# Kernel optimization log

Measured on AMD Instinct MI355X. Metric: run time of the kernel, lower is better.

The kernel has to match this reference:

```python
import jax, jax.numpy as jnp
import numpy as np

H = 12  # num_heads (init kwarg)


def setup_inputs() -> dict:
    key = jax.random.key(0)
    ks = jax.random.split(key, 9)
    B, S, D, M = 2, 1025, 768, 4
    hw = S - 1
    x = jax.random.normal(ks[0], (B, S, D), dtype=jnp.float32)
    masks = jax.random.randint(ks[1], (B, M, hw), 0, 2, dtype=jnp.int32)
    init = lambda k: jax.random.normal(k, (D, D), dtype=jnp.float32) * 0.02
    return {
        'x': x, 'masks': masks,
        'Wq': init(ks[2]), 'bq': jnp.zeros((D,), jnp.float32),
        'Wk': init(ks[3]), 'bk': jnp.zeros((D,), jnp.float32),
        'Wv': init(ks[4]), 'bv': jnp.zeros((D,), jnp.float32),
    }


def reference(x, masks, Wq, bq, Wk, bk, Wv, bv):
    B, S, D = x.shape
    hd = D // H
    scale = 1.0 / jnp.sqrt(jnp.asarray(hd, x.dtype))

    def heads(t):  # (B,S,D) -> (B,H,S,hd)
        return t.reshape(B, S, H, hd).transpose(0, 2, 1, 3)

    q = heads(x @ Wq.T + bq)
    k = heads(x @ Wk.T + bk)
    v = heads(x @ Wv.T + bv)

    scores_ori = jnp.einsum('bhqd,bhkd->bhqk', q, k) * scale  # (B,H,S,S)
    attn = jax.nn.softmax(scores_ori, axis=-1)  # dropout is identity at eval
    h = jnp.einsum('bhqk,bhkd->bhqd', attn, v)
    h = h.transpose(0, 2, 1, 3).reshape(B, S, D)

    # ---- mask-expanded attention (torch.no_grad branch) ----
    Mk, hw = masks.shape[1], masks.shape[2]
    m = masks.astype(x.dtype)  # (B,M,hw)
    # pad: position 0 (CLS) gets 0, positions 1..hw get the mask
    new_masks = jnp.pad(m, ((0, 0), (0, 0), (1, S - 1 - hw)))  # (B,M,S)
    bias = -10000.0 * (1.0 - new_masks)  # additive mask bias
    new_scores = scores_ori[:, None] + bias[:, :, None, None, :]  # (B,M,H,S,S)
    new_attn = jax.nn.softmax(new_scores, axis=-1)
    new_h = jnp.einsum('bmhqk,bhkd->bmhqd', new_attn, v)  # v repeated per mask
    new_h = new_h.transpose(0, 1, 3, 2, 4).reshape(B * Mk, S, D)

    img_idx = jnp.repeat(jnp.arange(B), Mk)  # [0]*M + [1]*M + ...
    new_x = jnp.broadcast_to(x[:, None], (B, Mk, S, D)).reshape(B * Mk, S, D)
    return (h, new_h, img_idx, new_x)
```

## Files before the change

### kernel.cpp

```cpp
#include <hip/hip_runtime.h>

typedef float f32x4 __attribute__((ext_vector_type(4)));
typedef short s16x8 __attribute__((ext_vector_type(8)));

constexpr int B  = 2;
constexpr int S  = 1025;
constexpr int D  = 768;
constexpr int DD = D * D;
constexpr int H  = 12;
constexpr int NM = 4;
constexpr int ROWS = B * S;
constexpr int BSD  = B * S * D;
constexpr int KPAD = 1088;
constexpr int NHB  = B * H;
constexpr int NQT  = 65;
constexpr int NKT  = 17;
constexpr int NV5  = 5;
constexpr int NATT = NHB * NQT;
constexpr int NCPY = 512;
constexpr int OUT_NEWH_OFF = BSD;
constexpr int OUT_IDX_OFF  = BSD + NM * BSD;
constexpr int OUT_NEWX_OFF = OUT_IDX_OFF + B * NM;

#define QSCALE 0.18033688011112042f

constexpr size_t QF_SZ = (size_t)NHB * NQT * 2 * 512;
constexpr size_t KF_SZ = (size_t)NHB * NKT * 4 * 2 * 512;
constexpr size_t VF_SZ = KF_SZ;

__device__ __forceinline__ unsigned short f2bf(float f) {
    unsigned u = __builtin_bit_cast(unsigned, f);
    u += 0x7FFF + ((u >> 16) & 1);
    return (unsigned short)(u >> 16);
}

__device__ __forceinline__ void gll16(const void* g, void* l) {
    __builtin_amdgcn_global_load_lds(
        (const __attribute__((address_space(1))) void*)g,
        (__attribute__((address_space(3))) void*)l, 16, 0, 0);
}

__global__ __launch_bounds__(256) void conv_kernel(
    const float* __restrict__ x, const float* __restrict__ Wq,
    const float* __restrict__ Wk, const float* __restrict__ Wv,
    const int* __restrict__ masks,
    unsigned short* __restrict__ xb, unsigned short* __restrict__ Wb,
    unsigned short* __restrict__ Mmb,
    unsigned short* __restrict__ Qf, unsigned short* __restrict__ Kf,
    unsigned short* __restrict__ Vf)
{
    constexpr int NX8 = BSD / 8;
    constexpr int NW8 = DD / 8;
    constexpr int TOT = NX8 + 3 * NW8;
    const int stride = gridDim.x * 256;
    const int tid = blockIdx.x * 256 + threadIdx.x;
    for (int c = tid; c < TOT; c += stride) {
        const float* src;
        unsigned short* dst;
        if (c < NX8) { src = x + (size_t)c * 8; dst = xb + (size_t)c * 8; }
        else {
            const int cc = c - NX8;
            const int mt = cc / NW8;
            const int rr = cc - mt * NW8;
            src = ((mt == 0) ? Wq : (mt == 1) ? Wk : Wv) + (size_t)rr * 8;
            dst = Wb + (size_t)mt * DD + (size_t)rr * 8;
        }
        const float4 a = *(const float4*)src;
        const float4 b2 = *(const float4*)(src + 4);
        s16x8 v;
        v[0] = (short)f2bf(a.x);  v[1] = (short)f2bf(a.y);
        v[2] = (short)f2bf(a.z);  v[3] = (short)f2bf(a.w);
        v[4] = (short)f2bf(b2.x); v[5] = (short)f2bf(b2.y);
        v[6] = (short)f2bf(b2.z); v[7] = (short)f2bf(b2.w);
        *(s16x8*)dst = v;
    }
    if (tid < B * NV5 * KPAD) {
        const int k    = tid % KPAD;
        const int rest = tid / KPAD;
        const int vv   = rest % NV5;
        const int bb   = rest / NV5;
        unsigned short m;
        if (vv == 0) m = (k < S) ? 0xFFFFu : 0u;
        else m = (k >= 1 && k < S &&
                  masks[(size_t)(bb * NM + vv - 1) * (S - 1) + k - 1]) ? 0xFFFFu : 0u;
        Mmb[tid] = m;
    }
    constexpr int KZ = NHB * 8 * 512;
    for (int i = tid; i < KZ; i += stride) {
        const int hb = i >> 12, off = i & 4095;
        Kf[(((size_t)(hb * NKT + NKT - 1)) << 12) + off] = 0;
        Vf[(((size_t)(hb * NKT + NKT - 1)) << 12) + off] = 0;
    }
    constexpr int QZ = NHB * 2 * 512;
    for (int i = tid; i < QZ; i += stride) {
        const int hb = i >> 10, off = i & 1023;
        Qf[(((size_t)(hb * NQT + NQT - 1) * 2) << 9) + off] = 0;
    }
}

__global__ __launch_bounds__(256, 2) void qkv_mfma_kernel(
    const unsigned short* __restrict__ xb, const unsigned short* __restrict__ Wb,
    const float* __restrict__ bq, const float* __restrict__ bk,
    const float* __restrict__ bv,
    unsigned short* __restrict__ Qf, unsigned short* __restrict__ Kf,
    unsigned short* __restrict__ Vf)
{
    __shared__ __align__(16) unsigned short Xs[2][128 * 64];
    __shared__ __align__(16) unsigned short Wl[2][128 * 64];

    const int t = threadIdx.x;
    const int row0 = blockIdx.x * 128;
    const int cy = blockIdx.y;
    const int mt = cy / 6;
    const int col0 = (cy % 6) * 128;
    const float* bias = (mt == 0) ? bq : (mt == 1) ? bk : bv;
    const unsigned short* Wsrc = Wb + (size_t)mt * DD;

    const int w = t >> 6, l = t & 63, lq = l & 15, grp = l >> 4;
    const int wr = w >> 1, wc = w & 1;

    auto stage = [&](int buf, int k0) {
        #pragma unroll
        for (int i = 0; i < 4; ++i) {
            const int slot = i * 256 + t;
            const int r = slot >> 3, cl = slot & 7;
            const int cg = cl ^ (r & 7);
            int row = row0 + r; if (row > ROWS - 1) row = ROWS - 1;
            gll16(xb + (size_t)row * D + k0 + cg * 8, &Xs[buf][slot * 8]);
            gll16(Wsrc + (size_t)(col0 + r) * D + k0 + cg * 8, &Wl[buf][slot * 8]);
        }
    };

    f32x4 acc[4][4] = {};
    stage(0, 0);

    for (int ks = 0; ks < 12; ++ks) {
        const int cur = ks & 1;
        __syncthreads();
        if (ks + 1 < 12) stage(cur ^ 1, (ks + 1) * 64);

        s16x8 a[4][2], bf[4][2];
        #pragma unroll
        for (int i = 0; i < 4; ++i) {
            const int xr = wr * 64 + i * 16 + lq;
            #pragma unroll
            for (int kh = 0; kh < 2; ++kh)
                a[i][kh] = *(const s16x8*)&Xs[cur][xr * 64 + (((kh * 4 + grp) ^ (xr & 7)) * 8)];
        }
        #pragma unroll
        for (int j = 0; j < 4; ++j) {
            const int wrow = wc * 64 + j * 16 + lq;
            #pragma unroll
            for (int kh = 0; kh < 2; ++kh)
                bf[j][kh] = *(const s16x8*)&Wl[cur][wrow * 64 + (((kh * 4 + grp) ^ (wrow & 7)) * 8)];
        }
        #pragma unroll
        for (int i = 0; i < 4; ++i)
            #pragma unroll
            for (int j = 0; j < 4; ++j) {
                acc[i][j] = __builtin_amdgcn_mfma_f32_16x16x32_bf16(a[i][0], bf[j][0], acc[i][j], 0, 0, 0);
                acc[i][j] = __builtin_amdgcn_mfma_f32_16x16x32_bf16(a[i][1], bf[j][1], acc[i][j], 0, 0, 0);
            }
    }

    #pragma unroll
    for (int j = 0; j < 4; ++j) {
        const int col = col0 + wc * 64 + j * 16 + lq;
        const float bv_ = bias[col];
        #pragma unroll
        for (int i = 0; i < 4; ++i) {
            #pragma unroll
            for (int r = 0; r < 4; ++r) {
                const int row = row0 + wr * 64 + i * 16 + grp * 4 + r;
                if (row >= ROWS) continue;
                const float raw = acc[i][j][r] + bv_;
                const int bb = (row >= S) ? 1 : 0;
                const int s  = row - bb * S;
                const int hb2 = bb * H + (col >> 6);
                const int d   = col & 63;
                if (mt == 0) {
                    const size_t idx = (((size_t)(hb2 * NQT + (s >> 4)) * 2 + (d >> 5)) << 9)
                                     + (((((d >> 3) & 3) << 4) + (s & 15)) << 3) + (d & 7);
                    Qf[idx] = f2bf(raw * QSCALE);
                } else if (mt == 1) {
                    const size_t idx = ((((size_t)(hb2 * NKT + (s >> 6)) * 4 + ((s >> 4) & 3)) * 2 + (d >> 5)) << 9)
                                     + (((((d >> 3) & 3) << 4) + (s & 15)) << 3) + (d & 7);
                    Kf[idx] = f2bf(raw);
                } else {
                    const int kk = s & 63;
                    const size_t idx = ((((size_t)(hb2 * NKT + (s >> 6)) * 4 + (d >> 4)) * 2 + (kk >> 5)) << 9)
                                     + (((((kk >> 3) & 3) << 4) + (d & 15)) << 3) + (kk & 7);
                    Vf[idx] = f2bf(raw);
                }
            }
        }
    }
}

__global__ __launch_bounds__(384) void attn_mfma_kernel(
    const unsigned short* __restrict__ Qf, const unsigned short* __restrict__ Kf,
    const unsigned short* __restrict__ Vf, const unsigned short* __restrict__ Mmb,
    const float* __restrict__ x,
    float* __restrict__ out_h, float* __restrict__ out_newh,
    float* __restrict__ out_newx, float* __restrict__ out_idx)
{
    if (blockIdx.x >= NATT) {
        const int cb = blockIdx.x - NATT;
        const int SLAB4  = S * D / 4;
        const int TOTAL4 = B * NM * SLAB4;
        const float4* x4 = (const float4*)x;
        float4* o4 = (float4*)out_newx;
        for (int f = cb * 384 + threadIdx.x; f < TOTAL4; f += NCPY * 384) {
            const int bm  = f / SLAB4;
            const int rem = f - bm * SLAB4;
            o4[f] = x4[(bm >> 2) * SLAB4 + rem];
        }
        if (cb == 0 && threadIdx.x < B * NM)
            out_idx[threadIdx.x] = (float)(threadIdx.x >> 2);
        return;
    }

    __shared__ __align__(16) unsigned short KVl[2][2][4096];
    __shared__ __align__(16) unsigned short Pb2[2][1024];

    const int orig = blockIdx.x;
    const int wgid = (orig & 7) * 195 + (orig >> 3);
    const int hb = wgid / NQT;
    const int qt = wgid - hb * NQT;
    const int b  = hb / H, hh = hb - b * H;
    const int q0 = qt * 16;

    const int t = threadIdx.x;
    const int w = t >> 6, l = t & 63;
    const int lq = l & 15, grp = l >> 4;

    const unsigned short* kfT = Kf + (((size_t)(hb * NKT)) << 12);
    const unsigned short* vfT = Vf + (((size_t)(hb * NKT)) << 12);

    auto stage = [&](int buf, int tile) {
        const unsigned short* ks = kfT + ((size_t)tile << 12);
        const unsigned short* vs = vfT + ((size_t)tile << 12);
        #pragma unroll
        for (int i = 0; i < 3; ++i) {
            const int s = t + i * 384;
            if (s < 512)       gll16(ks + s * 8, &KVl[buf][0][s * 8]);
            else if (s < 1024) gll16(vs + (s - 512) * 8, &KVl[buf][1][(s - 512) * 8]);
        }
    };

    stage(0, 0);

    if (w == 0) {
        s16x8 qf0, qf1;
        {
            const unsigned short* p = Qf + (((size_t)(hb * NQT + qt) * 2) << 9) + (l << 3);
            qf0 = *(const s16x8*)p;
            qf1 = *(const s16x8*)(p + 512);
        }
        #pragma unroll
        for (int it = 0; it < NKT; ++it) {
            const int cur = it & 1;
            __syncthreads();
            if (it + 1 < NKT) stage(cur ^ 1, it + 1);

            s16x8 kf[4][2];
            #pragma unroll
            for (int kt = 0; kt < 4; ++kt)
                #pragma unroll
                for (int kh = 0; kh < 2; ++kh)
                    kf[kt][kh] = *(const s16x8*)&KVl[cur][0][((kt * 2 + kh) << 9) + l * 8];

            f32x4 qk[4] = {};
            __builtin_amdgcn_s_setprio(1);
            #pragma unroll
            for (int kt = 0; kt < 4; ++kt) {
                qk[kt] = __builtin_amdgcn_mfma_f32_16x16x32_bf16(kf[kt][0], qf0, qk[kt], 0, 0, 0);
                qk[kt] = __builtin_amdgcn_mfma_f32_16x16x32_bf16(kf[kt][1], qf1, qk[kt], 0, 0, 0);
            }
            __builtin_amdgcn_s_setprio(0);

            unsigned short* P = &Pb2[cur][0];
            #pragma unroll
            for (int kt = 0; kt < 4; ++kt) {
                float e0, e1, e2, e3;
                asm("v_exp_f32 %0, %1" : "=v"(e0) : "v"(qk[kt][0]));
                asm("v_exp_f32 %0, %1" : "=v"(e1) : "v"(qk[kt][1]));
                asm("v_exp_f32 %0, %1" : "=v"(e2) : "v"(qk[kt][2]));
                asm("v_exp_f32 %0, %1" : "=v"(e3) : "v"(qk[kt][3]));
                unsigned d0, d1;
                asm("v_cvt_pk_bf16_f32 %0, %1, %2" : "=v"(d0) : "v"(e0), "v"(e1));
                asm("v_cvt_pk_bf16_f32 %0, %1, %2" : "=v"(d1) : "v"(e2), "v"(e3));
                const int chunk = kt * 2 + (grp >> 1);
                *(uint2*)&P[lq * 64 + ((chunk ^ (lq & 7)) * 8) + (grp & 1) * 4] =
                    make_uint2(d0, d1);
            }
        }
        __syncthreads();
    } else {
        const int vv = w - 1;
        const unsigned short* mbase = Mmb + (size_t)(b * NV5 + vv) * KPAD + grp * 8;

        s16x8 onesf;
        #pragma unroll
        for (int i = 0; i < 8; ++i) onesf[i] = (short)0x3F80;

        f32x4 acc[5] = {};
        s16x8 vfp[4][2];
        s16x8 mmA0, mmA1;

        auto pv = [&](s16x8 ea0, s16x8 ea1, s16x8 mm0, s16x8 mm1) {
            s16x8 pa0 = ea0 & mm0;
            s16x8 pa1 = ea1 & mm1;
            __builtin_amdgcn_s_setprio(1);
            #pragma unroll
            for (int dt = 0; dt < 4; ++dt)
                acc[dt] = __builtin_amdgcn_mfma_f32_16x16x32_bf16(vfp[dt][0], pa0, acc[dt], 0, 0, 0);
            acc[4] = __builtin_amdgcn_mfma_f32_16x16x32_bf16(onesf, pa0, acc[4], 0, 0, 0);
            #pragma unroll
            for (int dt = 0; dt < 4; ++dt)
                acc[dt] = __builtin_amdgcn_mfma_f32_16x16x32_bf16(vfp[dt][1], pa1, acc[dt], 0, 0, 0);
            acc[4] = __builtin_amdgcn_mfma_f32_16x16x32_bf16(onesf, pa1, acc[4], 0, 0, 0);
            __builtin_amdgcn_s_setprio(0);
        };

        mmA0 = *(const s16x8*)(mbase + 0);
        mmA1 = *(const s16x8*)(mbase + 32);

        #pragma unroll
        for (int it = 0; it < NKT; ++it) {
            const int cur = it & 1;
            __syncthreads();
            if (it + 1 < NKT) stage(cur ^ 1, it + 1);

            s16x8 pr0, pr1;
            if (it > 0) {
                const unsigned short* Pr = &Pb2[cur ^ 1][0];
                pr0 = *(const s16x8*)&Pr[lq * 64 + ((grp ^ (lq & 7)) * 8)];
                pr1 = *(const s16x8*)&Pr[lq * 64 + (((4 + grp) ^ (lq & 7)) * 8)];
            }
            s16x8 vfc[4][2];
            #pragma unroll
            for (int dt = 0; dt < 4; ++dt)
                #pragma unroll
                for (int kh = 0; kh < 2; ++kh)
                    vfc[dt][kh] = *(const s16x8*)&KVl[cur][1][((dt * 2 + kh) << 9) + l * 8];
            s16x8 mmB0 = *(const s16x8*)(mbase + it * 64);
            s16x8 mmB1 = *(const s16x8*)(mbase + it * 64 + 32);

            if (it > 0) pv(pr0, pr1, mmA0, mmA1);

            #pragma unroll
            for (int dt = 0; dt < 4; ++dt) {
                vfp[dt][0] = vfc[dt][0];
                vfp[dt][1] = vfc[dt][1];
            }
            mmA0 = mmB0; mmA1 = mmB1;
        }
        __syncthreads();
        {
            const unsigned short* Pr = &Pb2[(NKT - 1) & 1][0];
            s16x8 pr0 = *(const s16x8*)&Pr[lq * 64 + ((grp ^ (lq & 7)) * 8)];
            s16x8 pr1 = *(const s16x8*)&Pr[lq * 64 + (((4 + grp) ^ (lq & 7)) * 8)];
            pv(pr0, pr1, mmA0, mmA1);
        }

        const int q = q0 + lq;
        if (q < S) {
            const float inv = 1.0f / acc[4][0];
            float* bp = ((vv == 0)
                ? out_h    + (size_t)(b * S + q) * D
                : out_newh + (size_t)((b * NM + vv - 1) * S + q) * D) + hh * 64 + grp * 4;
            #pragma unroll
            for (int dt = 0; dt < 4; ++dt) {
                float4 s4;
                s4.x = acc[dt][0] * inv; s4.y = acc[dt][1] * inv;
                s4.z = acc[dt][2] * inv; s4.w = acc[dt][3] * inv;
                *(float4*)(bp + dt * 16) = s4;
            }
        }
    }
}

extern "C" void kernel_launch(void* const* d_in, const int* in_sizes, int n_in,
                              void* d_out, int out_size, void* d_ws, size_t ws_size,
                              hipStream_t stream)
{
    const float* x     = (const float*)d_in[0];
    const int*   masks = (const int*)  d_in[1];
    const float* Wq    = (const float*)d_in[2];
    const float* bq    = (const float*)d_in[3];
    const float* Wk    = (const float*)d_in[4];
    const float* bk    = (const float*)d_in[5];
    const float* Wv    = (const float*)d_in[6];
    const float* bv    = (const float*)d_in[7];

    float* out = (float*)d_out;
    float* out_h    = out;
    float* out_newh = out + OUT_NEWH_OFF;
    float* out_idx  = out + OUT_IDX_OFF;
    float* out_newx = out + OUT_NEWX_OFF;

    unsigned short* Qf  = (unsigned short*)d_ws;
    unsigned short* Kf  = Qf + QF_SZ;
    unsigned short* Vf  = Kf + KF_SZ;
    unsigned short* Mmb = Vf + VF_SZ;

    unsigned short* xb = (unsigned short*)out_newx;
    unsigned short* Wb = xb + BSD;

    conv_kernel<<<1634, 256, 0, stream>>>(x, Wq, Wk, Wv, masks, xb, Wb, Mmb,
                                          Qf, Kf, Vf);
    {
        dim3 grid(17, 18);
        qkv_mfma_kernel<<<grid, 256, 0, stream>>>(xb, Wb, bq, bk, bv, Qf, Kf, Vf);
    }
    attn_mfma_kernel<<<NATT + NCPY, 384, 0, stream>>>(Qf, Kf, Vf, Mmb, x,
                                                      out_h, out_newh,
                                                      out_newx, out_idx);
}
```

Baseline: 93.61 us.

## Shrink QKV GEMM tiles and move new_x copy into QKV kernel

The QKV projection GEMM now uses 64x128 tiles instead of 128x128, in a flattened 1D grid of 594 blocks. Each wave computes a 64x32 slice, which gives more blocks across the CUs. The broadcast copy of x into new_x and the img_idx write move from the attention kernel to extra blocks in the QKV launch, so they overlap with the GEMM rather than competing with attention. The bf16 scratch for x and W moves from the new_x region to the new_h region, since new_x is now written concurrently. Smaller tiles mean less operand reuse per block and more repeated W loads.

```diff
diff --git a/kernel.cpp b/kernel.cpp
--- a/kernel.cpp
+++ b/kernel.cpp
@@ -17,6 +17,7 @@
 constexpr int NKT  = 17;
 constexpr int NV5  = 5;
 constexpr int NATT = NHB * NQT;
+constexpr int NQKV = 33 * 18;
 constexpr int NCPY = 512;
 constexpr int OUT_NEWH_OFF = BSD;
 constexpr int OUT_IDX_OFF  = BSD + NM * BSD;
@@ -103,35 +104,59 @@
     const float* __restrict__ bq, const float* __restrict__ bk,
     const float* __restrict__ bv,
     unsigned short* __restrict__ Qf, unsigned short* __restrict__ Kf,
-    unsigned short* __restrict__ Vf)
+    unsigned short* __restrict__ Vf,
+    const float* __restrict__ x,
+    float* __restrict__ out_newx, float* __restrict__ out_idx)
 {
-    __shared__ __align__(16) unsigned short Xs[2][128 * 64];
+    if (blockIdx.x >= NQKV) {
+        const int cb = blockIdx.x - NQKV;
+        const int SLAB4  = S * D / 4;
+        const int TOTAL4 = B * NM * SLAB4;
+        const float4* x4 = (const float4*)x;
+        float4* o4 = (float4*)out_newx;
+        for (int f = cb * 256 + threadIdx.x; f < TOTAL4; f += NCPY * 256) {
+            const int bm  = f / SLAB4;
+            const int rem = f - bm * SLAB4;
+            o4[f] = x4[(bm >> 2) * SLAB4 + rem];
+        }
+        if (cb == 0 && threadIdx.x < B * NM)
+            out_idx[threadIdx.x] = (float)(threadIdx.x >> 2);
+        return;
+    }
+
+    __shared__ __align__(16) unsigned short Xs[2][64 * 64];
     __shared__ __align__(16) unsigned short Wl[2][128 * 64];
 
     const int t = threadIdx.x;
-    const int row0 = blockIdx.x * 128;
-    const int cy = blockIdx.y;
+    const int bx = blockIdx.x % 33;
+    const int cy = blockIdx.x / 33;
+    const int row0 = bx * 64;
     const int mt = cy / 6;
     const int col0 = (cy % 6) * 128;
     const float* bias = (mt == 0) ? bq : (mt == 1) ? bk : bv;
     const unsigned short* Wsrc = Wb + (size_t)mt * DD;
 
     const int w = t >> 6, l = t & 63, lq = l & 15, grp = l >> 4;
-    const int wr = w >> 1, wc = w & 1;
 
     auto stage = [&](int buf, int k0) {
         #pragma unroll
-        for (int i = 0; i < 4; ++i) {
+        for (int i = 0; i < 2; ++i) {
             const int slot = i * 256 + t;
             const int r = slot >> 3, cl = slot & 7;
             const int cg = cl ^ (r & 7);
             int row = row0 + r; if (row > ROWS - 1) row = ROWS - 1;
             gll16(xb + (size_t)row * D + k0 + cg * 8, &Xs[buf][slot * 8]);
+        }
+        #pragma unroll
+        for (int i = 0; i < 4; ++i) {
+            const int slot = i * 256 + t;
+            const int r = slot >> 3, cl = slot & 7;
+            const int cg = cl ^ (r & 7);
             gll16(Wsrc + (size_t)(col0 + r) * D + k0 + cg * 8, &Wl[buf][slot * 8]);
         }
     };
 
-    f32x4 acc[4][4] = {};
+    f32x4 acc[4][2] = {};
     stage(0, 0);
 
     for (int ks = 0; ks < 12; ++ks) {
@@ -139,17 +164,17 @@
         __syncthreads();
         if (ks + 1 < 12) stage(cur ^ 1, (ks + 1) * 64);
 
-        s16x8 a[4][2], bf[4][2];
+        s16x8 a[4][2], bf[2][2];
         #pragma unroll
         for (int i = 0; i < 4; ++i) {
-            const int xr = wr * 64 + i * 16 + lq;
+            const int xr = i * 16 + lq;
             #pragma unroll
             for (int kh = 0; kh < 2; ++kh)
                 a[i][kh] = *(const s16x8*)&Xs[cur][xr * 64 + (((kh * 4 + grp) ^ (xr & 7)) * 8)];
         }
         #pragma unroll
-        for (int j = 0; j < 4; ++j) {
-            const int wrow = wc * 64 + j * 16 + lq;
+        for (int j = 0; j < 2; ++j) {
+            const int wrow = w * 32 + j * 16 + lq;
             #pragma unroll
             for (int kh = 0; kh < 2; ++kh)
                 bf[j][kh] = *(const s16x8*)&Wl[cur][wrow * 64 + (((kh * 4 + grp) ^ (wrow & 7)) * 8)];
@@ -157,21 +182,21 @@
         #pragma unroll
         for (int i = 0; i < 4; ++i)
             #pragma unroll
-            for (int j = 0; j < 4; ++j) {
+            for (int j = 0; j < 2; ++j) {
                 acc[i][j] = __builtin_amdgcn_mfma_f32_16x16x32_bf16(a[i][0], bf[j][0], acc[i][j], 0, 0, 0);
                 acc[i][j] = __builtin_amdgcn_mfma_f32_16x16x32_bf16(a[i][1], bf[j][1], acc[i][j], 0, 0, 0);
             }
     }
 
     #pragma unroll
-    for (int j = 0; j < 4; ++j) {
-        const int col = col0 + wc * 64 + j * 16 + lq;
+    for (int j = 0; j < 2; ++j) {
+        const int col = col0 + w * 32 + j * 16 + lq;
         const float bv_ = bias[col];
         #pragma unroll
         for (int i = 0; i < 4; ++i) {
             #pragma unroll
             for (int r = 0; r < 4; ++r) {
-                const int row = row0 + wr * 64 + i * 16 + grp * 4 + r;
+                const int row = row0 + i * 16 + grp * 4 + r;
                 if (row >= ROWS) continue;
                 const float raw = acc[i][j][r] + bv_;
                 const int bb = (row >= S) ? 1 : 0;
@@ -200,26 +225,8 @@
 __global__ __launch_bounds__(384) void attn_mfma_kernel(
     const unsigned short* __restrict__ Qf, const unsigned short* __restrict__ Kf,
     const unsigned short* __restrict__ Vf, const unsigned short* __restrict__ Mmb,
-    const float* __restrict__ x,
-    float* __restrict__ out_h, float* __restrict__ out_newh,
-    float* __restrict__ out_newx, float* __restrict__ out_idx)
+    float* __restrict__ out_h, float* __restrict__ out_newh)
 {
-    if (blockIdx.x >= NATT) {
-        const int cb = blockIdx.x - NATT;
-        const int SLAB4  = S * D / 4;
-        const int TOTAL4 = B * NM * SLAB4;
-        const float4* x4 = (const float4*)x;
-        float4* o4 = (float4*)out_newx;
-        for (int f = cb * 384 + threadIdx.x; f < TOTAL4; f += NCPY * 384) {
-            const int bm  = f / SLAB4;
-            const int rem = f - bm * SLAB4;
-            o4[f] = x4[(bm >> 2) * SLAB4 + rem];
-        }
-        if (cb == 0 && threadIdx.x < B * NM)
-            out_idx[threadIdx.x] = (float)(threadIdx.x >> 2);
-        return;
-    }
-
     __shared__ __align__(16) unsigned short KVl[2][2][4096];
     __shared__ __align__(16) unsigned short Pb2[2][1024];
 
@@ -405,16 +412,14 @@
     unsigned short* Vf  = Kf + KF_SZ;
     unsigned short* Mmb = Vf + VF_SZ;
 
-    unsigned short* xb = (unsigned short*)out_newx;
+    unsigned short* xb = (unsigned short*)out_newh;
     unsigned short* Wb = xb + BSD;
 
     conv_kernel<<<1634, 256, 0, stream>>>(x, Wq, Wk, Wv, masks, xb, Wb, Mmb,
                                           Qf, Kf, Vf);
-    {
-        dim3 grid(17, 18);
-        qkv_mfma_kernel<<<grid, 256, 0, stream>>>(xb, Wb, bq, bk, bv, Qf, Kf, Vf);
-    }
-    attn_mfma_kernel<<<NATT + NCPY, 384, 0, stream>>>(Qf, Kf, Vf, Mmb, x,
-                                                      out_h, out_newh,
-                                                      out_newx, out_idx);
-}
+    qkv_mfma_kernel<<<NQKV + NCPY, 256, 0, stream>>>(xb, Wb, bq, bk, bv,
+                                                     Qf, Kf, Vf,
+                                                     x, out_newx, out_idx);
+    attn_mfma_kernel<<<NATT, 384, 0, stream>>>(Qf, Kf, Vf, Mmb,
+                                               out_h, out_newh);
+}
```

Measured after the change: 83.30 us, median of 2. -11.0%, faster.
